# Kernel optimization log

Measured on AMD Instinct MI355X. Metric: run time of the kernel, lower is better.

## Reference

```python
import jax, jax.numpy as jnp
import numpy as np

LOOKUP_WINDOW = 101
OUTPUT_DIM = 128
NUM_BINS = 512


def setup_inputs() -> dict:
    key = jax.random.key(0)
    k1, k2 = jax.random.split(key)
    frames = jax.random.randint(k1, (16, 100, 27, 48, 3), 0, 256, dtype=jnp.int32)
    fc_w = jax.random.normal(k2, (LOOKUP_WINDOW, OUTPUT_DIM), dtype=jnp.float32) * 0.05
    fc_b = jnp.zeros((OUTPUT_DIM,), dtype=jnp.float32)
    return {"frames": frames, "fc_w": fc_w, "fc_b": fc_b}


def _color_histograms(frames):
    # frames: [B, T, H, W, 3] int32 in [0, 256)
    B, T, H, W, C = frames.shape
    f = frames.reshape(B * T, H * W, 3)
    R, G, Bc = f[:, :, 0], f[:, :, 1], f[:, :, 2]
    # 3 bits per channel -> 512 bins
    bins = ((R >> 5) << 6) + ((G >> 5) << 3) + (Bc >> 5)  # [BT, HW]
    frame_prefix = (jnp.arange(B * T, dtype=jnp.int32) << 9)[:, None]
    ids = (bins + frame_prefix).reshape(-1)
    hist = jax.ops.segment_sum(
        jnp.ones_like(ids, dtype=jnp.int32), ids,
        num_segments=B * T * NUM_BINS)
    hist = hist.reshape(B, T, NUM_BINS).astype(jnp.float32)
    # L2-normalize each frame's histogram
    hist = hist / jnp.linalg.norm(hist, axis=2, keepdims=True)
    return hist


def reference(frames, fc_w, fc_b):
    B, T = frames.shape[0], frames.shape[1]
    x = _color_histograms(frames)                  # [B, T, 512]
    sim = jnp.einsum('btd,bsd->bts', x, x)         # [B, T, T]
    half = (LOOKUP_WINDOW - 1) // 2
    padded = jnp.pad(sim, ((0, 0), (0, 0), (half, half)))  # [B, T, T+lw-1]
    # banded gather: band[b, t, w] = padded[b, t, t + w]
    idx = jnp.arange(T)[:, None] + jnp.arange(LOOKUP_WINDOW)[None, :]  # [T, lw]
    band = jnp.take_along_axis(
        padded, jnp.broadcast_to(idx[None], (B, T, LOOKUP_WINDOW)), axis=2)
    # Dense + relu
    return jax.nn.relu(band @ fc_w + fc_b)         # [B, T, 128]
```

## Files before the change

### kernel.cpp

```cpp
#include <hip/hip_runtime.h>
#include <hip/hip_bf16.h>
#include <math.h>

#define B_DIM 16
#define T_DIM 100
#define TPAD 112
#define HW_PIX (27 * 48)
#define NBINS 512
#define WIN 101
#define HALF 50
#define ODIM 128
#define NTILE 7
#define SSTRIDE 132

typedef __attribute__((ext_vector_type(8))) short s16x8;
typedef __attribute__((ext_vector_type(4))) float f32x4;

__global__ __launch_bounds__(256) void hist_kernel(
    const int* __restrict__ frames, __hip_bfloat16* __restrict__ X16) {
  const int bid = blockIdx.x;
  const int tid = threadIdx.x;
  const int b = bid / T_DIM;
  const int t = bid - b * T_DIM;

  __shared__ int h[NBINS];
  __shared__ float red[16];

  for (int i = tid; i < NBINS; i += 256) h[i] = 0;

  if (t == 0) {
    unsigned int* zr = (unsigned int*)(X16 + ((size_t)(b * TPAD + T_DIM)) * NBINS);
    zr[tid] = 0u;
  }
  __syncthreads();

  const int* fp = frames + (size_t)bid * (HW_PIX * 3);
  for (int i = tid; i < HW_PIX / 4; i += 256) {
    const int4* q = (const int4*)(fp + 12 * i);
    int4 a = q[0], c = q[1], e = q[2];
    int b0 = ((a.x >> 5) << 6) + ((a.y >> 5) << 3) + (a.z >> 5);
    int b1 = ((a.w >> 5) << 6) + ((c.x >> 5) << 3) + (c.y >> 5);
    int b2 = ((c.z >> 5) << 6) + ((c.w >> 5) << 3) + (e.x >> 5);
    int b3 = ((e.y >> 5) << 6) + ((e.z >> 5) << 3) + (e.w >> 5);
    atomicAdd(&h[b0], 1);
    atomicAdd(&h[b1], 1);
    atomicAdd(&h[b2], 1);
    atomicAdd(&h[b3], 1);
  }
  __syncthreads();

  float ss = 0.f;
  for (int i = tid; i < NBINS; i += 256) {
    float v = (float)h[i];
    ss += v * v;
  }
  const int lane = tid & 63, wave = tid >> 6;
#pragma unroll
  for (int off = 32; off > 0; off >>= 1) ss += __shfl_down(ss, off);
  if (lane == 0) red[wave] = ss;
  __syncthreads();
  if (tid == 0) red[8] = 1.0f / sqrtf(red[0] + red[1] + red[2] + red[3]);
  __syncthreads();
  const float rn = red[8];

  {
    unsigned int lo = (unsigned int)__bfloat16_as_ushort(
        __float2bfloat16((float)h[2 * tid] * rn));
    unsigned int hi = (unsigned int)__bfloat16_as_ushort(
        __float2bfloat16((float)h[2 * tid + 1] * rn));
    unsigned int* row =
        (unsigned int*)(X16 + ((size_t)(b * TPAD + t)) * NBINS);
    row[tid] = lo | (hi << 16);
  }
}

__global__ __launch_bounds__(256) void simfc_kernel(
    const __hip_bfloat16* __restrict__ X16, const float* __restrict__ fc_w,
    const float* __restrict__ fc_b, float* __restrict__ out) {
  __shared__ __align__(16) float wlds[WIN * ODIM];
  __shared__ __align__(16) float slds[16 * SSTRIDE];

  const int cid = blockIdx.x;
  const int b = cid / NTILE;
  const int t0 = (cid - b * NTILE) * 16;
  const int tid = threadIdx.x;

  {
    const f32x4* src = (const f32x4*)fc_w;
    f32x4* dst = (f32x4*)wlds;
    for (int i = tid; i < (WIN * ODIM) / 4; i += 256) dst[i] = src[i];
  }

  const int lane = tid & 63, wv = tid >> 6;
  const int m16 = lane & 15, quad = lane >> 4;

  const short* Abase =
      (const short*)(X16 + ((size_t)(b * TPAD + t0 + m16)) * NBINS) + quad * 8;
  const short* zrow =
      (const short*)(X16 + ((size_t)(b * TPAD + T_DIM)) * NBINS) + quad * 8;

  const int s0 = t0 - HALF + wv * 32 + m16;
  const int s1 = s0 + 16;
  const short* B0 = (s0 >= 0 && s0 < T_DIM)
      ? (const short*)(X16 + ((size_t)(b * TPAD + s0)) * NBINS) + quad * 8
      : zrow;
  const short* B1 = (s1 >= 0 && s1 < T_DIM)
      ? (const short*)(X16 + ((size_t)(b * TPAD + s1)) * NBINS) + quad * 8
      : zrow;

  f32x4 acc0 = {0.f, 0.f, 0.f, 0.f};
  f32x4 acc1 = {0.f, 0.f, 0.f, 0.f};
#pragma unroll 8
  for (int k = 0; k < NBINS; k += 32) {
    s16x8 af = *(const s16x8*)(Abase + k);
    s16x8 bf0 = *(const s16x8*)(B0 + k);
    s16x8 bf1 = *(const s16x8*)(B1 + k);
    acc0 = __builtin_amdgcn_mfma_f32_16x16x32_bf16(af, bf0, acc0, 0, 0, 0);
    acc1 = __builtin_amdgcn_mfma_f32_16x16x32_bf16(af, bf1, acc1, 0, 0, 0);
  }

#pragma unroll
  for (int r = 0; r < 4; ++r) {
    slds[(quad * 4 + r) * SSTRIDE + wv * 32 + m16] = acc0[r];
    slds[(quad * 4 + r) * SSTRIDE + wv * 32 + 16 + m16] = acc1[r];
  }
  __syncthreads();

  const int g4 = tid & 31;
  const int tl0 = tid >> 5;
  const int tl1 = tl0 + 8;

  f32x4 accA = ((const f32x4*)fc_b)[g4];
  f32x4 accB = accA;
#pragma unroll 4
  for (int j = 0; j < WIN; ++j) {
    f32x4 w4 = *(const f32x4*)&wlds[j * ODIM + g4 * 4];
    float v0 = slds[tl0 * SSTRIDE + tl0 + j];
    float v1 = slds[tl1 * SSTRIDE + tl1 + j];
    accA += w4 * v0;
    accB += w4 * v1;
  }

#pragma unroll
  for (int c = 0; c < 4; ++c) {
    accA[c] = fmaxf(accA[c], 0.f);
    accB[c] = fmaxf(accB[c], 0.f);
  }

  const int ta = t0 + tl0, tb = t0 + tl1;
  if (ta < T_DIM)
    *(f32x4*)&out[((size_t)b * T_DIM + ta) * ODIM + g4 * 4] = accA;
  if (tb < T_DIM)
    *(f32x4*)&out[((size_t)b * T_DIM + tb) * ODIM + g4 * 4] = accB;
}

extern "C" void kernel_launch(void* const* d_in, const int* in_sizes, int n_in,
                              void* d_out, int out_size, void* d_ws, size_t ws_size,
                              hipStream_t stream) {
  const int* frames = (const int*)d_in[0];
  const float* fc_w = (const float*)d_in[1];
  const float* fc_b = (const float*)d_in[2];
  float* out = (float*)d_out;

  __hip_bfloat16* X16 = (__hip_bfloat16*)d_ws;

  hist_kernel<<<B_DIM * T_DIM, 256, 0, stream>>>(frames, X16);
  simfc_kernel<<<B_DIM * NTILE, 256, 0, stream>>>(X16, fc_w, fc_b, out);
}
```

Before: 85.53 us.

## Fuse histogram and similarity-FC kernels into one cooperative launch with grid sync

```diff
diff --git a/kernel.cpp b/kernel.cpp
--- a/kernel.cpp
+++ b/kernel.cpp
@@ -1,6 +1,9 @@
 #include <hip/hip_runtime.h>
 #include <hip/hip_bf16.h>
+#include <hip/hip_cooperative_groups.h>
 #include <math.h>
+
+namespace cg = cooperative_groups;
 
 #define B_DIM 16
 #define T_DIM 100
@@ -12,86 +15,95 @@
 #define ODIM 128
 #define NTILE 7
 #define SSTRIDE 132
+#define NBLOCKS 512
+#define NFRAMES (B_DIM * T_DIM)
 
 typedef __attribute__((ext_vector_type(8))) short s16x8;
 typedef __attribute__((ext_vector_type(4))) float f32x4;
 
-__global__ __launch_bounds__(256) void hist_kernel(
-    const int* __restrict__ frames, __hip_bfloat16* __restrict__ X16) {
+__global__ __launch_bounds__(256, 2) void fused_kernel(
+    const int* __restrict__ frames, const float* __restrict__ fc_w,
+    const float* __restrict__ fc_b, float* __restrict__ out,
+    __hip_bfloat16* __restrict__ X16) {
+  __shared__ __align__(16) unsigned char smem[WIN * ODIM * 4 + 16 * SSTRIDE * 4];
+  float* wlds = (float*)smem;
+  float* slds = (float*)(smem + WIN * ODIM * 4);
+
   const int bid = blockIdx.x;
   const int tid = threadIdx.x;
-  const int b = bid / T_DIM;
-  const int t = bid - b * T_DIM;
+  const int lane = tid & 63, wv = tid >> 6;
 
-  __shared__ int h[NBINS];
-  __shared__ float red[16];
+  {
+    int* hw = (int*)smem + wv * NBINS;
+    const int gwave = bid * 4 + wv;
 
-  for (int i = tid; i < NBINS; i += 256) h[i] = 0;
+    if (gwave < NFRAMES) {
+#pragma unroll
+      for (int k = 0; k < 8; ++k) hw[lane + 64 * k] = 0;
 
-  if (t == 0) {
-    unsigned int* zr = (unsigned int*)(X16 + ((size_t)(b * TPAD + T_DIM)) * NBINS);
-    zr[tid] = 0u;
+      const int* fp = frames + (size_t)gwave * (HW_PIX * 3);
+      for (int g = lane; g < HW_PIX / 4; g += 64) {
+        const int4* q = (const int4*)(fp + 12 * g);
+        int4 a = q[0], c = q[1], e = q[2];
+        int b0 = ((a.x >> 5) << 6) + ((a.y >> 5) << 3) + (a.z >> 5);
+        int b1 = ((a.w >> 5) << 6) + ((c.x >> 5) << 3) + (c.y >> 5);
+        int b2 = ((c.z >> 5) << 6) + ((c.w >> 5) << 3) + (e.x >> 5);
+        int b3 = ((e.y >> 5) << 6) + ((e.z >> 5) << 3) + (e.w >> 5);
+        atomicAdd(&hw[b0], 1);
+        atomicAdd(&hw[b1], 1);
+        atomicAdd(&hw[b2], 1);
+        atomicAdd(&hw[b3], 1);
+      }
+
+      float ss = 0.f;
+#pragma unroll
+      for (int k = 0; k < 8; ++k) {
+        float v = (float)hw[lane + 64 * k];
+        ss += v * v;
+      }
+#pragma unroll
+      for (int off = 32; off > 0; off >>= 1) ss += __shfl_xor(ss, off);
+      const float rn = 1.0f / sqrtf(ss);
+
+      const int b = gwave / T_DIM;
+      const int t = gwave - b * T_DIM;
+      unsigned int* row = (unsigned int*)(X16 + ((size_t)(b * TPAD + t)) * NBINS);
+      const int2* h2 = (const int2*)hw;
+#pragma unroll
+      for (int k = 0; k < 4; ++k) {
+        int i = lane + 64 * k;
+        int2 p = h2[i];
+        unsigned int lo = (unsigned int)__bfloat16_as_ushort(
+            __float2bfloat16((float)p.x * rn));
+        unsigned int hi = (unsigned int)__bfloat16_as_ushort(
+            __float2bfloat16((float)p.y * rn));
+        row[i] = lo | (hi << 16);
+      }
+    } else if (gwave < NFRAMES + B_DIM) {
+      const int b = gwave - NFRAMES;
+      unsigned int* zr = (unsigned int*)(X16 + ((size_t)(b * TPAD + T_DIM)) * NBINS);
+#pragma unroll
+      for (int k = 0; k < 4; ++k) zr[lane + 64 * k] = 0u;
+    }
   }
+
   __syncthreads();
 
-  const int* fp = frames + (size_t)bid * (HW_PIX * 3);
-  for (int i = tid; i < HW_PIX / 4; i += 256) {
-    const int4* q = (const int4*)(fp + 12 * i);
-    int4 a = q[0], c = q[1], e = q[2];
-    int b0 = ((a.x >> 5) << 6) + ((a.y >> 5) << 3) + (a.z >> 5);
-    int b1 = ((a.w >> 5) << 6) + ((c.x >> 5) << 3) + (c.y >> 5);
-    int b2 = ((c.z >> 5) << 6) + ((c.w >> 5) << 3) + (e.x >> 5);
-    int b3 = ((e.y >> 5) << 6) + ((e.z >> 5) << 3) + (e.w >> 5);
-    atomicAdd(&h[b0], 1);
-    atomicAdd(&h[b1], 1);
-    atomicAdd(&h[b2], 1);
-    atomicAdd(&h[b3], 1);
-  }
-  __syncthreads();
+  const bool worker = (bid < B_DIM * NTILE);
 
-  float ss = 0.f;
-  for (int i = tid; i < NBINS; i += 256) {
-    float v = (float)h[i];
-    ss += v * v;
-  }
-  const int lane = tid & 63, wave = tid >> 6;
-#pragma unroll
-  for (int off = 32; off > 0; off >>= 1) ss += __shfl_down(ss, off);
-  if (lane == 0) red[wave] = ss;
-  __syncthreads();
-  if (tid == 0) red[8] = 1.0f / sqrtf(red[0] + red[1] + red[2] + red[3]);
-  __syncthreads();
-  const float rn = red[8];
-
-  {
-    unsigned int lo = (unsigned int)__bfloat16_as_ushort(
-        __float2bfloat16((float)h[2 * tid] * rn));
-    unsigned int hi = (unsigned int)__bfloat16_as_ushort(
-        __float2bfloat16((float)h[2 * tid + 1] * rn));
-    unsigned int* row =
-        (unsigned int*)(X16 + ((size_t)(b * TPAD + t)) * NBINS);
-    row[tid] = lo | (hi << 16);
-  }
-}
-
-__global__ __launch_bounds__(256) void simfc_kernel(
-    const __hip_bfloat16* __restrict__ X16, const float* __restrict__ fc_w,
-    const float* __restrict__ fc_b, float* __restrict__ out) {
-  __shared__ __align__(16) float wlds[WIN * ODIM];
-  __shared__ __align__(16) float slds[16 * SSTRIDE];
-
-  const int cid = blockIdx.x;
-  const int b = cid / NTILE;
-  const int t0 = (cid - b * NTILE) * 16;
-  const int tid = threadIdx.x;
-
-  {
+  if (worker) {
     const f32x4* src = (const f32x4*)fc_w;
     f32x4* dst = (f32x4*)wlds;
     for (int i = tid; i < (WIN * ODIM) / 4; i += 256) dst[i] = src[i];
   }
 
-  const int lane = tid & 63, wv = tid >> 6;
+  __threadfence();
+  cg::this_grid().sync();
+
+  if (!worker) return;
+
+  const int b = bid / NTILE;
+  const int t0 = (bid - b * NTILE) * 16;
   const int m16 = lane & 15, quad = lane >> 4;
 
   const short* Abase =
@@ -161,9 +173,10 @@
   const float* fc_w = (const float*)d_in[1];
   const float* fc_b = (const float*)d_in[2];
   float* out = (float*)d_out;
-
   __hip_bfloat16* X16 = (__hip_bfloat16*)d_ws;
 
-  hist_kernel<<<B_DIM * T_DIM, 256, 0, stream>>>(frames, X16);
-  simfc_kernel<<<B_DIM * NTILE, 256, 0, stream>>>(X16, fc_w, fc_b, out);
+  void* args[] = {(void*)&frames, (void*)&fc_w, (void*)&fc_b, (void*)&out,
+                  (void*)&X16};
+  hipLaunchCooperativeKernel((void*)fused_kernel, dim3(NBLOCKS), dim3(256),
+                             args, 0, stream);
 }
```

After: 195.6 us. +128.7%, slower.
